# Optimization experiments

Hardware: AMD Instinct MI355X
Metric: run time of the kernel (lower is better)

The kernel has to match this reference:

```python
import jax, jax.numpy as jnp
import numpy as np

NEG_SLOPE = 0.01  # nn.LeakyReLU default
EPS = 1e-5        # nn.LayerNorm default


def _layernorm(x):
    # parameter-free LayerNorm over last dim (source calls nn.LayerNorm() with no shape)
    mu = jnp.mean(x, axis=-1, keepdims=True)
    var = jnp.var(x, axis=-1, keepdims=True)
    return (x - mu) * jax.lax.rsqrt(var + EPS)


def _leaky_relu(x):
    return jnp.where(x >= 0, x, NEG_SLOPE * x)


def setup_inputs() -> dict:
    key = jax.random.key(0)
    ks = jax.random.split(key, 9)
    B, N, F_IN, F_HID, HEADS, F_OUT = 8, 1024, 384, 96, 8, 384
    s_v = 1.0 / np.sqrt(F_IN)
    s_qk = 1.0 / np.sqrt(F_HID)
    s_m = 1.0 / np.sqrt(F_HID * HEADS + F_IN)
    return {
        "X": jax.random.normal(ks[0], (B, N, F_IN), jnp.float32),
        "Wv": jax.random.uniform(ks[1], (F_IN, F_HID), jnp.float32, -s_v, s_v),
        "bv": jax.random.uniform(ks[2], (F_HID,), jnp.float32, -s_v, s_v),
        "Wq": jax.random.uniform(ks[3], (F_HID, HEADS), jnp.float32, -s_qk, s_qk),
        "bq": jax.random.uniform(ks[4], (HEADS,), jnp.float32, -s_qk, s_qk),
        "Wk": jax.random.uniform(ks[5], (F_HID, HEADS), jnp.float32, -s_qk, s_qk),
        "bk": jax.random.uniform(ks[6], (HEADS,), jnp.float32, -s_qk, s_qk),
        "Wm": jax.random.uniform(ks[7], (F_HID * HEADS + F_IN, F_OUT), jnp.float32, -s_m, s_m),
        "bm": jax.random.uniform(ks[8], (F_OUT,), jnp.float32, -s_m, s_m),
    }


def reference(X, Wv, bv, Wq, bq, Wk, bk, Wm, bm):
    B, N, _ = X.shape
    Hn = _layernorm(X)
    # MultiHeadGraphAtten
    V = Hn @ Wv + bv                      # [B, N, f_hid]
    Q = V @ Wq + bq                       # [B, N, heads]
    K = V @ Wk + bk                       # [B, N, heads]
    A = _leaky_relu(jnp.einsum('bih,bjh->bijh', Q, K))  # [B, N, N, heads]
    A = jax.nn.softmax(A, axis=3)         # softmax over heads (dim=3), faithful to source
    Hh = jnp.einsum('bijh,bjf->bihf', A, V)  # [B, N, heads, f_hid]
    H = Hh.reshape(B, N, -1)              # [B, N, heads*f_hid]
    H = jnp.concatenate([H, X], axis=2)   # residual concat
    O = _layernorm(H) @ Wm + bm
    O = _leaky_relu(O)                    # dropout is identity in eval
    return jnp.concatenate([O, H], axis=2)
```

## Files before the change

### kernel.cpp

```cpp
#include <hip/hip_runtime.h>
#include <hip/hip_bf16.h>
#include <math.h>

#define BB 8
#define NN 1024
#define F_IN 384
#define F_HID 96
#define HEADS 8
#define F_OUT 384
#define ROWS (BB*NN)
#define H_DIM 1152
#define OUT_DIM 1536
#define NEG 0.01f
#define LN_EPS 1e-5f
#define LOG2E 1.4426950408889634f

typedef __bf16 bf16x8 __attribute__((ext_vector_type(8)));
typedef float  f32x4  __attribute__((ext_vector_type(4)));

static __device__ __forceinline__ unsigned short b16u(float x) {
    union { __bf16 h; unsigned short u; } c; c.h = (__bf16)x; return c.u;
}
static __device__ __forceinline__ unsigned int pk2(float lo, float hi) {
    return (unsigned int)b16u(lo) | ((unsigned int)b16u(hi) << 16);
}

typedef __attribute__((address_space(1))) const unsigned char g1_t;
typedef __attribute__((address_space(3))) unsigned char l3_t;
static __device__ __forceinline__ void gl16(const void* g, void* l) {
    __builtin_amdgcn_global_load_lds((g1_t*)g, (l3_t*)l, 16, 0, 0);
}

__global__ __launch_bounds__(256) void kW(const float* __restrict__ Wm,
                                          const float* __restrict__ Wv,
                                          unsigned short* __restrict__ WmT,
                                          unsigned short* __restrict__ WvT) {
    __shared__ float tile[32][33];
    const int t = threadIdx.x;
    const int bid = (int)blockIdx.x;
    const float* src; unsigned short* dst;
    int k0, n0, srcld, dstld;
    if (bid < 432) {
        k0 = (bid / 12) * 32; n0 = (bid % 12) * 32;
        src = Wm; dst = WmT; srcld = F_OUT; dstld = H_DIM;
    } else {
        const int e = bid - 432;
        k0 = (e / 3) * 32; n0 = (e % 3) * 32;
        src = Wv; dst = WvT; srcld = F_HID; dstld = F_IN;
    }
#pragma unroll
    for (int p = 0; p < 4; ++p) {
        const int e = t + 256*p, kk = e >> 5, nn = e & 31;
        tile[kk][nn] = src[(size_t)(k0 + kk) * srcld + n0 + nn];
    }
    __syncthreads();
#pragma unroll
    for (int p = 0; p < 4; ++p) {
        const int e = t + 256*p, nn = e >> 5, kk = e & 31;
        dst[(size_t)(n0 + nn) * dstld + k0 + kk] = b16u(tile[kk][nn]);
    }
}

__global__ __launch_bounds__(384) void kA(const float* __restrict__ X,
                                          const unsigned short* __restrict__ WvT,
                                          const float* __restrict__ bv,
                                          const float* __restrict__ Wq, const float* __restrict__ bq,
                                          const float* __restrict__ Wk, const float* __restrict__ bk,
                                          unsigned short* __restrict__ VT,
                                          float* __restrict__ Qw, float* __restrict__ Kw,
                                          float* __restrict__ out) {
    __shared__ __align__(16) unsigned short xn[16][392];
    __shared__ float vsh[96][17];
    const int t = threadIdx.x;
    const int bid = (int)blockIdx.x;
    const int swz = (bid & 7) * 64 + (bid >> 3);
    const int i0 = swz * 16;
    const int b = i0 >> 10, i_in = i0 & 1023;
    const int w = t >> 6, l = t & 63, m = l & 15, g = l >> 4;

    if (t < 256) {
        const int r = t >> 4, l16 = t & 15;
        const float4* xrow = (const float4*)(X + (size_t)(i0 + r) * F_IN);
        float4* oX = (float4*)(out + (size_t)(i0 + r) * OUT_DIM + F_OUT + HEADS*F_HID);
        float4 xv[6];
        float s = 0.f, sq = 0.f;
#pragma unroll
        for (int k = 0; k < 6; ++k) {
            xv[k] = xrow[l16 + 16*k];
            oX[l16 + 16*k] = xv[k];
            s  += xv[k].x + xv[k].y + xv[k].z + xv[k].w;
            sq += xv[k].x*xv[k].x + xv[k].y*xv[k].y + xv[k].z*xv[k].z + xv[k].w*xv[k].w;
        }
#pragma unroll
        for (int msk = 1; msk < 16; msk <<= 1) { s += __shfl_xor(s, msk); sq += __shfl_xor(sq, msk); }
        const float mu  = s * (1.f/F_IN);
        const float var = sq * (1.f/F_IN) - mu*mu;
        const float rstd = rsqrtf(var + LN_EPS);
#pragma unroll
        for (int k = 0; k < 6; ++k) {
            ushort4 h4;
            h4.x = b16u((xv[k].x - mu) * rstd);
            h4.y = b16u((xv[k].y - mu) * rstd);
            h4.z = b16u((xv[k].z - mu) * rstd);
            h4.w = b16u((xv[k].w - mu) * rstd);
            *(ushort4*)&xn[r][4*(l16 + 16*k)] = h4;
        }
    }
    __syncthreads();

    const f32x4 z4 = {0.f, 0.f, 0.f, 0.f};
    f32x4 acc = z4;
    const unsigned short* Br = WvT + (size_t)(w*16 + m) * F_IN + g*8;
#pragma unroll
    for (int ks = 0; ks < 12; ++ks) {
        const bf16x8 af  = *(const bf16x8*)&xn[m][ks*32 + g*8];
        const bf16x8 bfr = *(const bf16x8*)(Br + ks*32);
        acc = __builtin_amdgcn_mfma_f32_16x16x32_bf16(af, bfr, acc, 0, 0, 0);
    }
    {
        const int f = w*16 + m;
        const float bvv = bv[f];
#pragma unroll
        for (int r = 0; r < 4; ++r)
            vsh[f][g*4 + r] = acc[r] + bvv;
    }
    __syncthreads();

    {
        const int f = t >> 2, ic = (t & 3) * 4;
        ushort4 h4;
        h4.x = b16u(vsh[f][ic]);   h4.y = b16u(vsh[f][ic+1]);
        h4.z = b16u(vsh[f][ic+2]); h4.w = b16u(vsh[f][ic+3]);
        *(ushort4*)&VT[((size_t)b * F_HID + f) * NN + i_in + ic] = h4;
    }

    if (t < 256) {
        const int i_loc = t & 15, h = (t >> 4) & 7;
        const bool isQ = (t < 128);
        const float* Wx = isQ ? Wq : Wk;
        float a = isQ ? bq[h] : bk[h];
#pragma unroll 8
        for (int f = 0; f < F_HID; ++f)
            a = fmaf(vsh[f][i_loc], Wx[f*HEADS + h], a);
        if (isQ) Qw[(size_t)(i0 + i_loc) * HEADS + h] = a;
        else     Kw[(size_t)(i0 + i_loc) * HEADS + h] = a;
    }
}

__global__ __launch_bounds__(512, 4) void kB(const float* __restrict__ X,
                                             const unsigned short* __restrict__ VT,
                                             const float* __restrict__ Qw,
                                             const float* __restrict__ Kw,
                                             float* __restrict__ out,
                                             unsigned short* __restrict__ Hn) {
    __shared__ float q_sh[16][8];
    __shared__ float kT[2][HEADS][64];
    __shared__ __align__(16) unsigned short Wt[2][HEADS][16][64];
    __shared__ __align__(16) unsigned short vt_sh[2][F_HID][64];
    __shared__ float lnS[8][16], lnQ2[8][16];
    __shared__ float sxS[16], sx2S[16];
    __shared__ float mu_sh[16], rs_sh[16];

    const int t = threadIdx.x;
    const int bid = (int)blockIdx.x;
    const int swz = (bid & 7) * 64 + (bid >> 3);
    const int b  = swz >> 6;
    const int i0 = (swz & 63) * 16;
    const int w = t >> 6, l = t & 63, m = l & 15, g = l >> 4;
    const int hp = w >> 1, fh = w & 1;
    const int si = t >> 5, jd = t & 31;

    if (t < 128) ((float*)q_sh)[t] = Qw[((size_t)(b*NN + i0)) * HEADS + t];

    const f32x4 z4 = {0.f, 0.f, 0.f, 0.f};
    f32x4 acc[2][3];
#pragma unroll
    for (int h2 = 0; h2 < 2; ++h2)
#pragma unroll
        for (int fb = 0; fb < 3; ++fb) acc[h2][fb] = z4;

    const size_t vtbase = (size_t)b * F_HID * NN;
    const size_t krow   = (size_t)b * NN;

#define SMAX(kb, db)                                                                   \
    {                                                                                  \
        float2 kk[8];                                                                  \
        _Pragma("unroll")                                                              \
        for (int h = 0; h < 8; ++h)                                                    \
            kk[h] = *(const float2*)&kT[kb][h][2*jd];                                  \
        float p0[8], p1[8];                                                            \
        float s0 = 0.f, s1 = 0.f;                                                      \
        _Pragma("unroll")                                                              \
        for (int h = 0; h < 8; ++h) {                                                  \
            float a0 = q[h] * kk[h].x; a0 = fmaxf(a0, NEG*a0);                         \
            float a1 = q[h] * kk[h].y; a1 = fmaxf(a1, NEG*a1);                         \
            p0[h] = __builtin_amdgcn_exp2f(a0); s0 += p0[h];                           \
            p1[h] = __builtin_amdgcn_exp2f(a1); s1 += p1[h];                           \
        }                                                                              \
        const float inv0 = 1.f / s0, inv1 = 1.f / s1;                                  \
        char* wbase = (char*)Wt + (db)*16384 + si*128                                  \
                    + ((((jd>>2) ^ (si & 7))) << 4) + ((jd & 3) << 2);                 \
        _Pragma("unroll")                                                              \
        for (int h = 0; h < 8; ++h)                                                    \
            *(unsigned int*)(wbase + h*2048) = pk2(p0[h]*inv0, p1[h]*inv1);            \
    }

    {
        uint4 vr0, vr1;
        {
            const int f = t >> 3, u = t & 7;
            vr0 = *(const uint4*)(VT + vtbase + (size_t)f*NN + u*8);
        }
        if (t < 256) {
            const int e = t + 512, f2 = e >> 3, u2 = e & 7;
            vr1 = *(const uint4*)(VT + vtbase + (size_t)f2*NN + u2*8);
        }
        const float ka = Kw[(krow + l) * HEADS + w];
        const float kb_ = Kw[(krow + 64 + l) * HEADS + w];
        {
            const int f = t >> 3, u = t & 7;
            *(uint4*)((char*)vt_sh + f*128 + ((u ^ (f & 7)) << 4)) = vr0;
        }
        if (t < 256) {
            const int e = t + 512, f2 = e >> 3, u2 = e & 7;
            *(uint4*)((char*)vt_sh + f2*128 + ((u2 ^ (f2 & 7)) << 4)) = vr1;
        }
        kT[0][w][l] = ka;
        kT[1][w][l] = kb_;
    }
    __syncthreads();

    float q[8];
#pragma unroll
    for (int h = 0; h < 8; ++h) q[h] = q_sh[si][h] * LOG2E;

    SMAX(0, 0);
    __syncthreads();

    for (int c = 0; c < 16; ++c) {
        const int cur = c & 1, nxt = cur ^ 1;

        uint4 vr0, vr1; float kr = 0.f;
        if (c < 15) {
            const int j0n = (c + 1) * 64;
            {
                const int f = t >> 3, u = t & 7;
                vr0 = *(const uint4*)(VT + vtbase + (size_t)f*NN + j0n + u*8);
            }
            if (t < 256) {
                const int e = t + 512, f2 = e >> 3, u2 = e & 7;
                vr1 = *(const uint4*)(VT + vtbase + (size_t)f2*NN + j0n + u2*8);
            }
        }
        if (c < 14) kr = Kw[(krow + (size_t)(c + 2)*64 + l) * HEADS + w];

        if (c < 15) SMAX(nxt, nxt);

        __builtin_amdgcn_s_setprio(1);
#pragma unroll
        for (int kh = 0; kh < 2; ++kh) {
            const int swzu = ((kh*4 + g) ^ (m & 7)) << 4;
            bf16x8 af[2];
#pragma unroll
            for (int h2 = 0; h2 < 2; ++h2)
                af[h2] = *(const bf16x8*)((const char*)Wt + cur*16384
                                          + (hp*2 + h2)*2048 + m*128 + swzu);
            bf16x8 bfr[3];
#pragma unroll
            for (int fb = 0; fb < 3; ++fb) {
                const int f = fh*48 + fb*16 + m;
                bfr[fb] = *(const bf16x8*)((const char*)vt_sh + cur*12288 + f*128 + swzu);
            }
#pragma unroll
            for (int h2 = 0; h2 < 2; ++h2)
#pragma unroll
                for (int fb = 0; fb < 3; ++fb)
                    acc[h2][fb] = __builtin_amdgcn_mfma_f32_16x16x32_bf16(
                        af[h2], bfr[fb], acc[h2][fb], 0, 0, 0);
        }
        __builtin_amdgcn_s_setprio(0);

        if (c < 15) {
            {
                const int f = t >> 3, u = t & 7;
                *(uint4*)((char*)vt_sh + nxt*12288 + f*128 + ((u ^ (f & 7)) << 4)) = vr0;
            }
            if (t < 256) {
                const int e = t + 512, f2 = e >> 3, u2 = e & 7;
                *(uint4*)((char*)vt_sh + nxt*12288 + f2*128 + ((u2 ^ (f2 & 7)) << 4)) = vr1;
            }
        }
        if (c < 14) kT[cur][w][l] = kr;
        __syncthreads();
    }
#undef SMAX

    float s[4] = {0,0,0,0}, s2[4] = {0,0,0,0};
#pragma unroll
    for (int h2 = 0; h2 < 2; ++h2)
#pragma unroll
        for (int fb = 0; fb < 3; ++fb)
#pragma unroll
            for (int r = 0; r < 4; ++r) {
                const float v = acc[h2][fb][r];
                s[r] += v; s2[r] += v*v;
            }
#pragma unroll
    for (int msk = 1; msk < 16; msk <<= 1)
#pragma unroll
        for (int r = 0; r < 4; ++r) {
            s[r]  += __shfl_xor(s[r],  msk);
            s2[r] += __shfl_xor(s2[r], msk);
        }
    if (m == 0) {
#pragma unroll
        for (int r = 0; r < 4; ++r) { lnS[w][g*4+r] = s[r]; lnQ2[w][g*4+r] = s2[r]; }
    }

    const int rX = t >> 5, lX = t & 31;
    const size_t xrow = (size_t)(b*NN + i0 + rX);
    const float4* x4 = (const float4*)(X + xrow * F_IN);
    float4 xs[3];
    float sx = 0.f, sx2 = 0.f;
#pragma unroll
    for (int kk = 0; kk < 3; ++kk) {
        xs[kk] = x4[lX + 32*kk];
        sx  += xs[kk].x + xs[kk].y + xs[kk].z + xs[kk].w;
        sx2 += xs[kk].x*xs[kk].x + xs[kk].y*xs[kk].y + xs[kk].z*xs[kk].z + xs[kk].w*xs[kk].w;
    }
#pragma unroll
    for (int msk = 1; msk < 32; msk <<= 1) { sx += __shfl_xor(sx, msk); sx2 += __shfl_xor(sx2, msk); }
    if (lX == 0) { sxS[rX] = sx; sx2S[rX] = sx2; }
    __syncthreads();

    if (t < 16) {
        float tot = sxS[t], tot2 = sx2S[t];
#pragma unroll
        for (int ww = 0; ww < 8; ++ww) { tot += lnS[ww][t]; tot2 += lnQ2[ww][t]; }
        const float muh = tot * (1.f/H_DIM);
        const float varh = tot2 * (1.f/H_DIM) - muh*muh;
        mu_sh[t] = muh; rs_sh[t] = rsqrtf(varh + LN_EPS);
    }
    __syncthreads();

#pragma unroll
    for (int r = 0; r < 4; ++r) {
        const int row = g*4 + r;
        const size_t orow = (size_t)(b*NN + i0 + row);
        const float muh = mu_sh[row], rs = rs_sh[row];
#pragma unroll
        for (int h2 = 0; h2 < 2; ++h2)
#pragma unroll
            for (int fb = 0; fb < 3; ++fb) {
                const int col = (hp*2 + h2)*F_HID + fh*48 + fb*16 + m;
                const float v = acc[h2][fb][r];
                out[orow * OUT_DIM + F_OUT + col] = v;
                Hn[orow * H_DIM + col] = b16u((v - muh) * rs);
            }
    }
    {
        const float muh = mu_sh[rX], rs = rs_sh[rX];
#pragma unroll
        for (int kk = 0; kk < 3; ++kk) {
            ushort4 hh;
            hh.x = b16u((xs[kk].x - muh) * rs);
            hh.y = b16u((xs[kk].y - muh) * rs);
            hh.z = b16u((xs[kk].z - muh) * rs);
            hh.w = b16u((xs[kk].w - muh) * rs);
            *(ushort4*)&Hn[xrow * H_DIM + HEADS*F_HID + 4*(lX + 32*kk)] = hh;
        }
    }
}

__global__ __launch_bounds__(256) void kC(const unsigned short* __restrict__ Hn,
                                          const unsigned short* __restrict__ WmT,
                                          const float* __restrict__ bm,
                                          float* __restrict__ out) {
    __shared__ __align__(16) unsigned short As[2][64*64];
    __shared__ __align__(16) unsigned short Bs[2][48*64];
    const int t = threadIdx.x, w = t >> 6, lane = t & 63, m = lane & 15, g = lane >> 4;
    const int bid = (int)blockIdx.x;
    const int swz = (bid & 7) * 128 + (bid >> 3);
    const int i0 = (swz >> 3) * 64;
    const int n0 = (swz & 7) * 48;

    const f32x4 z4 = {0.f, 0.f, 0.f, 0.f};
    f32x4 acc[3];
#pragma unroll
    for (int ns = 0; ns < 3; ++ns) acc[ns] = z4;

#define KC_STAGE(buf, k0)                                                              \
    {                                                                                  \
        _Pragma("unroll")                                                              \
        for (int p = 0; p < 2; ++p) {                                                  \
            const int e = t + 256*p, row = e >> 3, c16 = e & 7;                        \
            gl16(Hn + (size_t)(i0+row)*H_DIM + (k0) + ((c16 ^ (row&7)) << 3),          \
                 (char*)As[buf] + e*16);                                               \
        }                                                                              \
        {                                                                              \
            const int row = t >> 3, c16 = t & 7;                                       \
            gl16(WmT + (size_t)(n0+row)*H_DIM + (k0) + ((c16 ^ (row&7)) << 3),         \
                 (char*)Bs[buf] + t*16);                                               \
        }                                                                              \
        if (t < 128) {                                                                 \
            const int e = t + 256, row = e >> 3, c16 = e & 7;                          \
            gl16(WmT + (size_t)(n0+row)*H_DIM + (k0) + ((c16 ^ (row&7)) << 3),         \
                 (char*)Bs[buf] + e*16);                                               \
        }                                                                              \
    }

    KC_STAGE(0, 0);
    __syncthreads();

    for (int s = 0; s < 18; ++s) {
        const int cur = s & 1;
        if (s < 17) KC_STAGE(cur ^ 1, (s + 1) * 64);
#pragma unroll
        for (int kh = 0; kh < 2; ++kh) {
            const int kb = kh*64 + g*16;
            const int rowA = w*16 + m;
            const bf16x8 af = *(const bf16x8*)((const char*)As[cur] + rowA*128
                                               + (kb ^ ((rowA&7)<<4)));
#pragma unroll
            for (int ns = 0; ns < 3; ++ns) {
                const int row = ns*16 + m;
                const bf16x8 bf_ = *(const bf16x8*)((const char*)Bs[cur] + row*128
                                                    + (kb ^ ((row&7)<<4)));
                acc[ns] = __builtin_amdgcn_mfma_f32_16x16x32_bf16(af, bf_, acc[ns], 0, 0, 0);
            }
        }
        __syncthreads();
    }
#undef KC_STAGE

#pragma unroll
    for (int ns = 0; ns < 3; ++ns) {
        const int col = n0 + ns*16 + m;
        const float bmv = bm[col];
#pragma unroll
        for (int r = 0; r < 4; ++r) {
            float o = acc[ns][r] + bmv;
            o = fmaxf(o, NEG * o);
            out[(size_t)(i0 + w*16 + g*4 + r) * OUT_DIM + col] = o;
        }
    }
}

extern "C" void kernel_launch(void* const* d_in, const int* in_sizes, int n_in,
                              void* d_out, int out_size, void* d_ws, size_t ws_size,
                              hipStream_t stream) {
    const float* X  = (const float*)d_in[0];
    const float* Wv = (const float*)d_in[1];
    const float* bv = (const float*)d_in[2];
    const float* Wq = (const float*)d_in[3];
    const float* bq = (const float*)d_in[4];
    const float* Wk = (const float*)d_in[5];
    const float* bk = (const float*)d_in[6];
    const float* Wm = (const float*)d_in[7];
    const float* bm = (const float*)d_in[8];
    float* out = (float*)d_out;

    char* p = (char*)d_ws;
    unsigned short* VT  = (unsigned short*)p;                 p += (size_t)BB*F_HID*NN*2;
    float*          Qw  = (float*)p;                          p += (size_t)ROWS*HEADS*4;
    float*          Kw  = (float*)p;                          p += (size_t)ROWS*HEADS*4;
    unsigned short* WmT = (unsigned short*)p;                 p += (size_t)F_OUT*H_DIM*2;
    unsigned short* WvT = (unsigned short*)p;                 p += (size_t)F_HID*F_IN*2;
    unsigned short* Hn  = (unsigned short*)p;
    (void)ws_size; (void)out_size; (void)n_in; (void)in_sizes;

    kW<<<468, 256, 0, stream>>>(Wm, Wv, WmT, WvT);
    kA<<<ROWS/16, 384, 0, stream>>>(X, WvT, bv, Wq, bq, Wk, bk, VT, Qw, Kw, out);
    kB<<<BB*(NN/16), 512, 0, stream>>>(X, VT, Qw, Kw, out, Hn);
    kC<<<(ROWS/64)*(F_OUT/48), 256, 0, stream>>>(Hn, WmT, bm, out);
}
```

Before: 72.03 us.

## Halve kB block to 256 threads with 32-wide j chunks and 4 heads per wave

The attention kernel now runs 256 threads per block instead of 512. It processes the j dimension in 32-wide chunks over 32 iterations instead of 64-wide over 16, and each wave accumulates 4 heads by 3 feature blocks of MFMA tiles. Shared-memory buffers, swizzles, softmax thread mapping and the LayerNorm reduction are resized to match. The aim is to cut LDS use and raise occupancy or per-wave MFMA reuse, at the cost of twice as many barriers per block and more accumulator registers per thread.

```diff
diff --git a/kernel.cpp b/kernel.cpp
--- a/kernel.cpp
+++ b/kernel.cpp
@@ -147,17 +147,17 @@
     }
 }
 
-__global__ __launch_bounds__(512, 4) void kB(const float* __restrict__ X,
+__global__ __launch_bounds__(256, 4) void kB(const float* __restrict__ X,
                                              const unsigned short* __restrict__ VT,
                                              const float* __restrict__ Qw,
                                              const float* __restrict__ Kw,
                                              float* __restrict__ out,
                                              unsigned short* __restrict__ Hn) {
+    __shared__ __align__(16) unsigned short Wt[2][HEADS][16][32];
+    __shared__ __align__(16) unsigned short vt_sh[2][F_HID][32];
+    __shared__ float kT[2][HEADS][32];
     __shared__ float q_sh[16][8];
-    __shared__ float kT[2][HEADS][64];
-    __shared__ __align__(16) unsigned short Wt[2][HEADS][16][64];
-    __shared__ __align__(16) unsigned short vt_sh[2][F_HID][64];
-    __shared__ float lnS[8][16], lnQ2[8][16];
+    __shared__ float lnS[4][16], lnQ2[4][16];
     __shared__ float sxS[16], sx2S[16];
     __shared__ float mu_sh[16], rs_sh[16];
 
@@ -167,15 +167,15 @@
     const int b  = swz >> 6;
     const int i0 = (swz & 63) * 16;
     const int w = t >> 6, l = t & 63, m = l & 15, g = l >> 4;
-    const int hp = w >> 1, fh = w & 1;
-    const int si = t >> 5, jd = t & 31;
+    const int hq = w & 1, fh = w >> 1;
+    const int si = t >> 4, jq = t & 15;
 
     if (t < 128) ((float*)q_sh)[t] = Qw[((size_t)(b*NN + i0)) * HEADS + t];
 
     const f32x4 z4 = {0.f, 0.f, 0.f, 0.f};
-    f32x4 acc[2][3];
-#pragma unroll
-    for (int h2 = 0; h2 < 2; ++h2)
+    f32x4 acc[4][3];
+#pragma unroll
+    for (int h2 = 0; h2 < 4; ++h2)
 #pragma unroll
         for (int fb = 0; fb < 3; ++fb) acc[h2][fb] = z4;
 
@@ -187,7 +187,7 @@
         float2 kk[8];                                                                  \
         _Pragma("unroll")                                                              \
         for (int h = 0; h < 8; ++h)                                                    \
-            kk[h] = *(const float2*)&kT[kb][h][2*jd];                                  \
+            kk[h] = *(const float2*)&kT[kb][h][2*jq];                                  \
         float p0[8], p1[8];                                                            \
         float s0 = 0.f, s1 = 0.f;                                                      \
         _Pragma("unroll")                                                              \
@@ -198,81 +198,72 @@
             p1[h] = __builtin_amdgcn_exp2f(a1); s1 += p1[h];                           \
         }                                                                              \
         const float inv0 = 1.f / s0, inv1 = 1.f / s1;                                  \
-        char* wbase = (char*)Wt + (db)*16384 + si*128                                  \
-                    + ((((jd>>2) ^ (si & 7))) << 4) + ((jd & 3) << 2);                 \
+        char* wbase = (char*)Wt + (db)*8192 + si*64                                    \
+                    + ((((jq>>2) ^ (si & 3))) << 4) + ((jq & 3) << 2);                 \
         _Pragma("unroll")                                                              \
         for (int h = 0; h < 8; ++h)                                                    \
-            *(unsigned int*)(wbase + h*2048) = pk2(p0[h]*inv0, p1[h]*inv1);            \
+            *(unsigned int*)(wbase + h*1024) = pk2(p0[h]*inv0, p1[h]*inv1);            \
     }
 
     {
-        uint4 vr0, vr1;
         {
-            const int f = t >> 3, u = t & 7;
-            vr0 = *(const uint4*)(VT + vtbase + (size_t)f*NN + u*8);
-        }
-        if (t < 256) {
-            const int e = t + 512, f2 = e >> 3, u2 = e & 7;
-            vr1 = *(const uint4*)(VT + vtbase + (size_t)f2*NN + u2*8);
-        }
-        const float ka = Kw[(krow + l) * HEADS + w];
-        const float kb_ = Kw[(krow + 64 + l) * HEADS + w];
+            const int f = t >> 2, u = t & 3;
+            const uint4 v = *(const uint4*)(VT + vtbase + (size_t)f*NN + u*8);
+            *(uint4*)((char*)vt_sh + f*64 + ((u ^ (f & 3)) << 4)) = v;
+        }
+        if (t < 128) {
+            const int e = t + 256, f = e >> 2, u = e & 3;
+            const uint4 v = *(const uint4*)(VT + vtbase + (size_t)f*NN + u*8);
+            *(uint4*)((char*)vt_sh + f*64 + ((u ^ (f & 3)) << 4)) = v;
+        }
+        const int hh = t >> 5, jj = t & 31;
+        kT[0][hh][jj] = Kw[(krow + jj) * HEADS + hh];
+        kT[1][hh][jj] = Kw[(krow + 32 + jj) * HEADS + hh];
+    }
+    __syncthreads();
+
+    float q[8];
+#pragma unroll
+    for (int h = 0; h < 8; ++h) q[h] = q_sh[si][h] * LOG2E;
+
+    SMAX(0, 0);
+    __syncthreads();
+
+    for (int c = 0; c < 32; ++c) {
+        const int cur = c & 1, nxt = cur ^ 1;
+
+        uint4 vr0, vr1; float kr = 0.f;
+        if (c < 31) {
+            const int j0n = (c + 1) * 32;
+            {
+                const int f = t >> 2, u = t & 3;
+                vr0 = *(const uint4*)(VT + vtbase + (size_t)f*NN + j0n + u*8);
+            }
+            if (t < 128) {
+                const int e = t + 256, f = e >> 2, u = e & 3;
+                vr1 = *(const uint4*)(VT + vtbase + (size_t)f*NN + j0n + u*8);
+            }
+        }
+        if (c < 30) kr = Kw[(krow + (size_t)(c + 2)*32 + (t & 31)) * HEADS + (t >> 5)];
+
+        if (c < 31) SMAX(nxt, nxt);
+
+        __builtin_amdgcn_s_setprio(1);
         {
-            const int f = t >> 3, u = t & 7;
-            *(uint4*)((char*)vt_sh + f*128 + ((u ^ (f & 7)) << 4)) = vr0;
-        }
-        if (t < 256) {
-            const int e = t + 512, f2 = e >> 3, u2 = e & 7;
-            *(uint4*)((char*)vt_sh + f2*128 + ((u2 ^ (f2 & 7)) << 4)) = vr1;
-        }
-        kT[0][w][l] = ka;
-        kT[1][w][l] = kb_;
-    }
-    __syncthreads();
-
-    float q[8];
-#pragma unroll
-    for (int h = 0; h < 8; ++h) q[h] = q_sh[si][h] * LOG2E;
-
-    SMAX(0, 0);
-    __syncthreads();
-
-    for (int c = 0; c < 16; ++c) {
-        const int cur = c & 1, nxt = cur ^ 1;
-
-        uint4 vr0, vr1; float kr = 0.f;
-        if (c < 15) {
-            const int j0n = (c + 1) * 64;
-            {
-                const int f = t >> 3, u = t & 7;
-                vr0 = *(const uint4*)(VT + vtbase + (size_t)f*NN + j0n + u*8);
-            }
-            if (t < 256) {
-                const int e = t + 512, f2 = e >> 3, u2 = e & 7;
-                vr1 = *(const uint4*)(VT + vtbase + (size_t)f2*NN + j0n + u2*8);
-            }
-        }
-        if (c < 14) kr = Kw[(krow + (size_t)(c + 2)*64 + l) * HEADS + w];
-
-        if (c < 15) SMAX(nxt, nxt);
-
-        __builtin_amdgcn_s_setprio(1);
-#pragma unroll
-        for (int kh = 0; kh < 2; ++kh) {
-            const int swzu = ((kh*4 + g) ^ (m & 7)) << 4;
-            bf16x8 af[2];
-#pragma unroll
-            for (int h2 = 0; h2 < 2; ++h2)
-                af[h2] = *(const bf16x8*)((const char*)Wt + cur*16384
-                                          + (hp*2 + h2)*2048 + m*128 + swzu);
+            const int swzu = (g ^ (m & 3)) << 4;
+            bf16x8 af[4];
+#pragma unroll
+            for (int h2 = 0; h2 < 4; ++h2)
+                af[h2] = *(const bf16x8*)((const char*)Wt + cur*8192
+                                          + (hq*4 + h2)*1024 + m*64 + swzu);
             bf16x8 bfr[3];
 #pragma unroll
             for (int fb = 0; fb < 3; ++fb) {
                 const int f = fh*48 + fb*16 + m;
-                bfr[fb] = *(const bf16x8*)((const char*)vt_sh + cur*12288 + f*128 + swzu);
-            }
-#pragma unroll
-            for (int h2 = 0; h2 < 2; ++h2)
+                bfr[fb] = *(const bf16x8*)((const char*)vt_sh + cur*6144 + f*64 + swzu);
+            }
+#pragma unroll
+            for (int h2 = 0; h2 < 4; ++h2)
 #pragma unroll
                 for (int fb = 0; fb < 3; ++fb)
                     acc[h2][fb] = __builtin_amdgcn_mfma_f32_16x16x32_bf16(
@@ -280,24 +271,24 @@
         }
         __builtin_amdgcn_s_setprio(0);
 
-        if (c < 15) {
+        if (c < 31) {
             {
-                const int f = t >> 3, u = t & 7;
-                *(uint4*)((char*)vt_sh + nxt*12288 + f*128 + ((u ^ (f & 7)) << 4)) = vr0;
-            }
-            if (t < 256) {
-                const int e = t + 512, f2 = e >> 3, u2 = e & 7;
-                *(uint4*)((char*)vt_sh + nxt*12288 + f2*128 + ((u2 ^ (f2 & 7)) << 4)) = vr1;
-            }
-        }
-        if (c < 14) kT[cur][w][l] = kr;
+                const int f = t >> 2, u = t & 3;
+                *(uint4*)((char*)vt_sh + nxt*6144 + f*64 + ((u ^ (f & 3)) << 4)) = vr0;
+            }
+            if (t < 128) {
+                const int e = t + 256, f = e >> 2, u = e & 3;
+                *(uint4*)((char*)vt_sh + nxt*6144 + f*64 + ((u ^ (f & 3)) << 4)) = vr1;
+            }
+        }
+        if (c < 30) kT[cur][t >> 5][t & 31] = kr;
         __syncthreads();
     }
 #undef SMAX
 
     float s[4] = {0,0,0,0}, s2[4] = {0,0,0,0};
 #pragma unroll
-    for (int h2 = 0; h2 < 2; ++h2)
+    for (int h2 = 0; h2 < 4; ++h2)
 #pragma unroll
         for (int fb = 0; fb < 3; ++fb)
 #pragma unroll
@@ -317,26 +308,26 @@
         for (int r = 0; r < 4; ++r) { lnS[w][g*4+r] = s[r]; lnQ2[w][g*4+r] = s2[r]; }
     }
 
-    const int rX = t >> 5, lX = t & 31;
+    const int rX = t >> 4, lX = t & 15;
     const size_t xrow = (size_t)(b*NN + i0 + rX);
     const float4* x4 = (const float4*)(X + xrow * F_IN);
-    float4 xs[3];
+    float4 xs[6];
     float sx = 0.f, sx2 = 0.f;
 #pragma unroll
-    for (int kk = 0; kk < 3; ++kk) {
-        xs[kk] = x4[lX + 32*kk];
+    for (int kk = 0; kk < 6; ++kk) {
+        xs[kk] = x4[lX + 16*kk];
         sx  += xs[kk].x + xs[kk].y + xs[kk].z + xs[kk].w;
         sx2 += xs[kk].x*xs[kk].x + xs[kk].y*xs[kk].y + xs[kk].z*xs[kk].z + xs[kk].w*xs[kk].w;
     }
 #pragma unroll
-    for (int msk = 1; msk < 32; msk <<= 1) { sx += __shfl_xor(sx, msk); sx2 += __shfl_xor(sx2, msk); }
+    for (int msk = 1; msk < 16; msk <<= 1) { sx += __shfl_xor(sx, msk); sx2 += __shfl_xor(sx2, msk); }
     if (lX == 0) { sxS[rX] = sx; sx2S[rX] = sx2; }
     __syncthreads();
 
     if (t < 16) {
         float tot = sxS[t], tot2 = sx2S[t];
 #pragma unroll
-        for (int ww = 0; ww < 8; ++ww) { tot += lnS[ww][t]; tot2 += lnQ2[ww][t]; }
+        for (int ww = 0; ww < 4; ++ww) { tot += lnS[ww][t]; tot2 += lnQ2[ww][t]; }
         const float muh = tot * (1.f/H_DIM);
         const float varh = tot2 * (1.f/H_DIM) - muh*muh;
         mu_sh[t] = muh; rs_sh[t] = rsqrtf(varh + LN_EPS);
@@ -349,10 +340,10 @@
         const size_t orow = (size_t)(b*NN + i0 + row);
         const float muh = mu_sh[row], rs = rs_sh[row];
 #pragma unroll
-        for (int h2 = 0; h2 < 2; ++h2)
+        for (int h2 = 0; h2 < 4; ++h2)
 #pragma unroll
             for (int fb = 0; fb < 3; ++fb) {
-                const int col = (hp*2 + h2)*F_HID + fh*48 + fb*16 + m;
+                const int col = (hq*4 + h2)*F_HID + fh*48 + fb*16 + m;
                 const float v = acc[h2][fb][r];
                 out[orow * OUT_DIM + F_OUT + col] = v;
                 Hn[orow * H_DIM + col] = b16u((v - muh) * rs);
@@ -361,13 +352,13 @@
     {
         const float muh = mu_sh[rX], rs = rs_sh[rX];
 #pragma unroll
-        for (int kk = 0; kk < 3; ++kk) {
+        for (int kk = 0; kk < 6; ++kk) {
             ushort4 hh;
             hh.x = b16u((xs[kk].x - muh) * rs);
             hh.y = b16u((xs[kk].y - muh) * rs);
             hh.z = b16u((xs[kk].z - muh) * rs);
             hh.w = b16u((xs[kk].w - muh) * rs);
-            *(ushort4*)&Hn[xrow * H_DIM + HEADS*F_HID + 4*(lX + 32*kk)] = hh;
+            *(ushort4*)&Hn[xrow * H_DIM + HEADS*F_HID + 4*(lX + 16*kk)] = hh;
         }
     }
 }
@@ -471,6 +462,6 @@
 
     kW<<<468, 256, 0, stream>>>(Wm, Wv, WmT, WvT);
     kA<<<ROWS/16, 384, 0, stream>>>(X, WvT, bv, Wq, bq, Wk, bk, VT, Qw, Kw, out);
-    kB<<<BB*(NN/16), 512, 0, stream>>>(X, VT, Qw, Kw, out, Hn);
+    kB<<<BB*(NN/16), 256, 0, stream>>>(X, VT, Qw, Kw, out, Hn);
     kC<<<(ROWS/64)*(F_OUT/48), 256, 0, stream>>>(Hn, WmT, bm, out);
 }
```

Result: slower. 74.59 us (+3.6%).
